# Kernel tuning notes

Hardware: AMD Instinct MI355X
Metric: run time of the kernel (lower is better)

Reference implementation:

```python
import jax, jax.numpy as jnp
import numpy as np

BINS = 2048
DST_NBINS = 8
STEP = 1e-5


def _get_norm(delta_begin, delta_end, density):
    # integral of x^2 * density over [delta_begin, delta_end]
    return density * (delta_end ** 3 - delta_begin ** 3) / 3.0


def _quant_error(hist, bin_width, nsb, neb):
    # L2 quantization error of mapping src bins [nsb, neb] onto DST_NBINS bins
    dst_w = bin_width * (neb - nsb + 1).astype(jnp.float32) / DST_NBINS
    safe_w = jnp.where(dst_w == 0.0, 1.0, dst_w)
    src = jnp.arange(BINS, dtype=jnp.float32)
    begin = (src - nsb) * bin_width          # src bin left edge rel. to new range
    end = begin + bin_width
    db = jnp.clip(jnp.floor(begin / safe_w), 0, DST_NBINS - 1)
    de = jnp.clip(jnp.floor(end / safe_w), 0, DST_NBINS - 1)
    density = hist / bin_width
    db_c = (db + 0.5) * safe_w
    norm = _get_norm(begin - db_c, safe_w / 2, density)
    norm = norm + (de - db - 1.0) * _get_norm(-safe_w / 2, safe_w / 2, density)
    de_c = de * safe_w + safe_w / 2
    norm = norm + _get_norm(-safe_w / 2, end - de_c, density)
    return jnp.where(dst_w == 0.0, jnp.float32(0.0), norm.sum())


def _search(hist, min_val, max_val):
    # entropy-style greedy shrink of [start_bin, end_bin]; sequential, data-dependent
    bin_width = (max_val - min_val) / BINS
    total = hist.sum()
    cSum = jnp.cumsum(hist)

    def cond(s):
        alpha, beta, sb, eb, nm, done = s
        return (alpha < beta) & jnp.logical_not(done)

    def body(s):
        alpha, beta, sb, eb, nm, done = s
        na = alpha + STEP
        nb = beta - STEP
        # l: first bin (>= sb) with cSum >= na*total; r: last bin with cSum <= nb*total
        l = jnp.clip(jnp.searchsorted(cSum, na * total, side='left'), sb, eb)
        r = jnp.clip(jnp.searchsorted(cSum, nb * total, side='right') - 1, sb, eb)
        take_left = (l - sb) > (eb - r)
        nsb = jnp.where(take_left, l, sb)
        neb = jnp.where(take_left, eb, r)
        alpha2 = jnp.where(take_left, na, alpha)
        beta2 = jnp.where(take_left, beta, nb)
        changed = (nsb != sb) | (neb != eb)
        norm = _quant_error(hist, bin_width, nsb, neb)
        broke = changed & (norm > nm)
        accept = changed & jnp.logical_not(broke)
        return (alpha2, beta2,
                jnp.where(accept, nsb, sb),
                jnp.where(accept, neb, eb),
                jnp.where(accept, norm, nm),
                done | broke)

    init = (jnp.float32(0.0), jnp.float32(1.0),
            jnp.int32(0), jnp.int32(BINS - 1),
            jnp.float32(jnp.inf), jnp.bool_(False))
    _, _, sb, eb, _, _ = jax.lax.while_loop(cond, body, init)
    return sb, eb


def _forward(x):
    min_val = jnp.min(x)
    max_val = jnp.max(x)
    bin_width = (max_val - min_val) / BINS
    safe_bw = jnp.where(bin_width == 0.0, 1.0, bin_width)
    # torch.histc equivalent over [min_val, max_val]
    idx = jnp.clip(jnp.floor((x.ravel() - min_val) / safe_bw).astype(jnp.int32), 0, BINS - 1)
    hist = jnp.zeros(BINS, jnp.float32).at[idx].add(1.0)
    sb, eb = _search(jax.lax.stop_gradient(hist),
                     jax.lax.stop_gradient(min_val),
                     jax.lax.stop_gradient(max_val))
    new_min = min_val + bin_width * sb
    new_max = min_val + bin_width * (eb + 1)
    return jnp.stack([new_min, new_max])


def setup_inputs() -> dict:
    key = jax.random.key(0)
    x = jax.random.normal(key, (32, 1024, 1024), dtype=jnp.float32)
    return {"x": x}


def reference(x):
    return _forward(x)
```

## Files before the change

### kernel.cpp

```cpp
#include <hip/hip_runtime.h>
#include <float.h>
#include <math.h>

#define BINS 2048
#define DSTN 8
#define STEPF 1e-5f
#define NPART 1024
#define MAXST 2048
#define NSEG 64
#define MINF 0x7fffffff

struct Ws {
  float pmin[NPART];
  float pmax[NPART];
  float min_val, max_val, bin_width, safe_bw;
  int   n_states;
  int   pad[3];
  unsigned int hist[BINS];
  float histf[BINS];
  float norms[MAXST];
  int2  states[MAXST];
};

__global__ void __launch_bounds__(256) k_minmax(const float* __restrict__ x, long long n,
                                                Ws* __restrict__ ws) {
  long long n4 = n >> 2;
  float vmin = FLT_MAX, vmax = -FLT_MAX;
  const float4* __restrict__ x4 = (const float4*)x;
  long long stride = (long long)gridDim.x * blockDim.x;
  for (long long i = (long long)blockIdx.x * blockDim.x + threadIdx.x; i < n4; i += stride) {
    float4 v = x4[i];
    vmin = fminf(vmin, fminf(fminf(v.x, v.y), fminf(v.z, v.w)));
    vmax = fmaxf(vmax, fmaxf(fmaxf(v.x, v.y), fmaxf(v.z, v.w)));
  }
  for (long long i = (n4 << 2) + (long long)blockIdx.x * blockDim.x + threadIdx.x; i < n; i += stride) {
    float v = x[i];
    vmin = fminf(vmin, v); vmax = fmaxf(vmax, v);
  }
  for (int off = 32; off > 0; off >>= 1) {
    vmin = fminf(vmin, __shfl_down(vmin, off));
    vmax = fmaxf(vmax, __shfl_down(vmax, off));
  }
  __shared__ float smin[4], smax[4];
  int wid = threadIdx.x >> 6;
  if ((threadIdx.x & 63) == 0) { smin[wid] = vmin; smax[wid] = vmax; }
  __syncthreads();
  if (threadIdx.x == 0) {
    float a = smin[0], b = smax[0];
    int nw = (int)(blockDim.x >> 6);
    for (int w = 1; w < nw; ++w) { a = fminf(a, smin[w]); b = fmaxf(b, smax[w]); }
    ws->pmin[blockIdx.x] = a; ws->pmax[blockIdx.x] = b;
  }
}

__global__ void __launch_bounds__(256) k_minmax_final(Ws* __restrict__ ws, int nparts) {
  __shared__ float smin[256], smax[256];
  int t = threadIdx.x;
  float vmin = FLT_MAX, vmax = -FLT_MAX;
  for (int i = t; i < nparts; i += 256) {
    vmin = fminf(vmin, ws->pmin[i]);
    vmax = fmaxf(vmax, ws->pmax[i]);
  }
  smin[t] = vmin; smax[t] = vmax;
  __syncthreads();
  for (int off = 128; off > 0; off >>= 1) {
    if (t < off) { smin[t] = fminf(smin[t], smin[t + off]); smax[t] = fmaxf(smax[t], smax[t + off]); }
    __syncthreads();
  }
  if (t == 0) {
    float mn = smin[0], mx = smax[0];
    ws->min_val = mn; ws->max_val = mx;
    float bw = (mx - mn) / (float)BINS;
    ws->bin_width = bw;
    ws->safe_bw = (bw == 0.0f) ? 1.0f : bw;
  }
  for (int i = t; i < BINS; i += 256) ws->hist[i] = 0u;
}

__global__ void __launch_bounds__(256) k_hist(const float* __restrict__ x, long long n,
                                              Ws* __restrict__ ws) {
  __shared__ unsigned int lh[BINS];
  for (int i = threadIdx.x; i < BINS; i += 256) lh[i] = 0u;
  __syncthreads();
  float minv = ws->min_val;
  float sbw = ws->safe_bw;
  long long n4 = n >> 2;
  const float4* __restrict__ x4 = (const float4*)x;
  long long stride = (long long)gridDim.x * blockDim.x;
  for (long long i = (long long)blockIdx.x * blockDim.x + threadIdx.x; i < n4; i += stride) {
    float4 v = x4[i];
    int a = (int)floorf((v.x - minv) / sbw);
    int b = (int)floorf((v.y - minv) / sbw);
    int c = (int)floorf((v.z - minv) / sbw);
    int d = (int)floorf((v.w - minv) / sbw);
    a = min(BINS - 1, max(0, a));
    b = min(BINS - 1, max(0, b));
    c = min(BINS - 1, max(0, c));
    d = min(BINS - 1, max(0, d));
    atomicAdd(&lh[a], 1u);
    atomicAdd(&lh[b], 1u);
    atomicAdd(&lh[c], 1u);
    atomicAdd(&lh[d], 1u);
  }
  for (long long i = (n4 << 2) + (long long)blockIdx.x * blockDim.x + threadIdx.x; i < n; i += stride) {
    int a = (int)floorf((x[i] - minv) / sbw);
    a = min(BINS - 1, max(0, a));
    atomicAdd(&lh[a], 1u);
  }
  __syncthreads();
  for (int i = threadIdx.x; i < BINS; i += 256) {
    unsigned int c = lh[i];
    if (c) atomicAdd(&ws->hist[i], c);
  }
}

__global__ void __launch_bounds__(256) k_search(Ws* __restrict__ ws) {
  __shared__ __align__(16) char arena[49216];
  float* csum   = (float*)(arena);
  float* Atab   = (float*)(arena + 8192);
  int2*  ev     = (int2*)(arena);
  int2*  ltmt   = (int2*)(arena + 16400);
  int*   mcross = (int*)(arena + 32816);
  int*   chain  = (int*)(arena + 41008);
  __shared__ __align__(16) int2 sstates[MAXST];
  __shared__ float part[256];
  __shared__ int   ipart[256];
  __shared__ int   ipart2[256];
  __shared__ __align__(16) int4 segB4[NSEG];
  __shared__ __align__(16) int4 segA4[NSEG];
  __shared__ int nseg_s, mbot_s, nsegA_s, nc_s;
  __shared__ int pub_mode, pub_j0, pub_sb, pub_mt, pub_nst0;

  int t = threadIdx.x;

  float loc[8];
  float s = 0.0f;
  #pragma unroll
  for (int kk = 0; kk < 8; ++kk) {
    float h = (float)ws->hist[t * 8 + kk];
    ws->histf[t * 8 + kk] = h;
    s += h;
    loc[kk] = s;
  }
  part[t] = s;
  __syncthreads();
  for (int off = 1; off < 256; off <<= 1) {
    float add = (t >= off) ? part[t - off] : 0.0f;
    __syncthreads();
    part[t] += add;
    __syncthreads();
  }
  float excl = (t == 0) ? 0.0f : part[t - 1];
  #pragma unroll
  for (int kk = 0; kk < 8; ++kk) csum[t * 8 + kk] = excl + loc[kk];
  __syncthreads();

  const float S = STEPF;
  const float T = csum[BINS - 1];
  const float rcpT = 1.0f / T;

  if (t == 0) {
    int sg = 0; float B = 1.0f; int m0 = 0; int mbot = MINF;
    while (sg < NSEG && B > 0.0f) {
      float Bn = B - S;
      if (Bn <= 0.0f) {
        segB4[sg] = make_int4(__float_as_int(B), __float_as_int(B - Bn), m0, 0);
        ++sg; mbot = m0 + 1; break;
      }
      float d = B - Bn;
      unsigned bb = __float_as_uint(B);
      unsigned bid = bb & 0x7f800000u;
      if ((bb & 0x007fffffu) == 0u) bid -= 0x00800000u;
      float binlo = __uint_as_float(bid);
      float brel = B - binlo;
      int n = (int)floor((double)brel / (double)d);
      if (n < 0) n = 0;
      if (n >= 2) {
        float B1 = B - d;
        float B2 = B1 - S;
        if (B1 - B2 != d) n = 1;
      }
      segB4[sg] = make_int4(__float_as_int(B), __float_as_int(d), m0, n);
      ++sg;
      float Blast = B - (float)n * d;
      B = Blast - S;
      m0 += n + 1;
      if (B <= 0.0f) { mbot = m0; break; }
    }
    nseg_s = sg; mbot_s = mbot;

    int sa = 0;
    segA4[sa++] = make_int4(__float_as_int(0.0f), __float_as_int(S), 0, 0);
    float A0 = S; int k0 = 1;
    while (sa < NSEG && k0 <= 2051) {
      float An = A0 + S;
      float d = An - A0;
      unsigned ab = __float_as_uint(A0);
      unsigned abid = ab & 0x7f800000u;
      float binhi = __uint_as_float(abid + 0x00800000u);
      float brel = binhi - A0;
      int n = (int)floorf(brel / d);
      if (n < 0) n = 0;
      while (n >= 1 && !(A0 + (float)n * d < binhi)) --n;
      while (A0 + (float)(n + 1) * d < binhi) ++n;
      if (n >= 2) {
        float A1 = A0 + d;
        float A2 = A1 + S;
        if (A2 - A1 != d) n = 1;
      }
      if (k0 + n > 2051) n = 2051 - k0;
      segA4[sa++] = make_int4(__float_as_int(A0), __float_as_int(d), k0, n);
      float Alast = A0 + (float)n * d;
      A0 = Alast + S;
      k0 += n + 1;
    }
    nsegA_s = sa;
  }
  __syncthreads();

  int nsg = nseg_s;
  int mbot = mbot_s;
  int nsa = nsegA_s;

  for (int k = t; k < 2052; k += 256) {
    float val = 0.0f;
    for (int sg = 0; sg < nsa; ++sg) {
      int4 sv = segA4[sg];
      if (k <= sv.z + sv.w) { val = __int_as_float(sv.x) + (float)(k - sv.z) * __int_as_float(sv.y); break; }
    }
    Atab[k] = val;
  }
  __syncthreads();

  {
    int okA = 1;
    for (int k = t; k < 2051; k += 256) okA &= (Atab[k] + S == Atab[k + 1]) ? 1 : 0;
    ipart[t] = okA;
    __syncthreads();
    for (int off = 128; off > 0; off >>= 1) {
      if (t < off) ipart[t] = min(ipart[t], ipart[t + off]);
      __syncthreads();
    }
    if (ipart[0] == 0) {
      if (t == 0) {
        float a = 0.0f; Atab[0] = 0.0f;
        for (int k = 1; k < 2052; ++k) { a = a + S; Atab[k] = a; }
      }
      __syncthreads();
    }
  }

  int lov[9], hiv[9];
  float av1[9];
  #pragma unroll
  for (int i = 0; i < 9; ++i) {
    int k = t + 256 * i;
    lov[i] = 0; hiv[i] = BINS;
    av1[i] = (k <= 2050) ? Atab[k + 1] * T : FLT_MAX;
  }
  #pragma unroll
  for (int lev = 0; lev < 12; ++lev) {
    #pragma unroll
    for (int i = 0; i < 9; ++i) {
      bool act = lov[i] < hiv[i];
      int mid = act ? ((lov[i] + hiv[i]) >> 1) : 0;
      float cv = csum[mid];
      bool g = act && (cv < av1[i]);
      lov[i] = g ? (mid + 1) : lov[i];
      hiv[i] = (act && !g) ? mid : hiv[i];
    }
  }
  #pragma unroll
  for (int i = 0; i < 9; ++i) {
    int k = t + 256 * i;
    if (k >= 2052) break;
    float a = Atab[k];
    int mt = mbot;
    for (int sg = 0; sg < nsg; ++sg) {
      int4 sv = segB4[sg];
      float Bs = __int_as_float(sv.x), dd = __int_as_float(sv.y);
      int ms = sv.z, n = sv.w;
      float Bend = Bs - (float)n * dd;
      if (Bend <= a) {
        float rd = (dd > 0.0f) ? 1.0f / dd : 0.0f;
        int i2 = (int)((Bs - a) * rd);
        if (i2 < 0) i2 = 0; if (i2 > n) i2 = n;
        while (i2 > 0 && Bs - (float)(i2 - 1) * dd <= a) --i2;
        while (i2 <= n && Bs - (float)i2 * dd > a) ++i2;
        mt = ms + i2;
        break;
      }
    }
    ltmt[k] = make_int2(lov[i], mt);
  }
  for (int b = t; b < BINS; b += 256) {
    float c = csum[b];
    int mc = MINF;
    if (c > 0.0f) {
      mc = (mbot == MINF) ? MINF : (mbot - 1);
      for (int sg = 0; sg < nsg; ++sg) {
        int4 sv = segB4[sg];
        float Bs = __int_as_float(sv.x), dd = __int_as_float(sv.y);
        int ms = sv.z, n = sv.w;
        float Bend = Bs - (float)n * dd;
        if (Bend * T < c) {
          float rd = (dd > 0.0f) ? 1.0f / dd : 0.0f;
          int i2 = (int)((Bs - c * rcpT) * rd);
          if (i2 < 0) i2 = 0; if (i2 > n) i2 = n;
          while (i2 > 0 && (Bs - (float)(i2 - 1) * dd) * T < c) --i2;
          while (i2 <= n && !((Bs - (float)i2 * dd) * T < c)) ++i2;
          mc = ms + i2 - 1;
          break;
        }
      }
    }
    mcross[b] = mc;
  }
  __syncthreads();

  int mcl[8];
  int iem = 0;
  {
    int b0 = t * 8;
    #pragma unroll
    for (int kk = 0; kk < 8; ++kk) mcl[kk] = mcross[b0 + kk];
    int mnext = (t < 255) ? mcross[b0 + 8] : 0;
    int cnt = 0;
    #pragma unroll
    for (int kk = 0; kk < 8; ++kk) {
      int nxtv = (kk < 7) ? mcl[kk + 1] : mnext;
      bool e = (b0 + kk == BINS - 1) || (mcl[kk] != nxtv);
      iem |= e ? (1 << kk) : 0;
      cnt += e ? 1 : 0;
    }
    ipart[t] = cnt;
  }
  __syncthreads();
  for (int off = 1; off < 256; off <<= 1) {
    int v = (t + off < 256) ? ipart[t + off] : 0;
    __syncthreads();
    ipart[t] += v;
    __syncthreads();
  }
  {
    int running = (t < 255) ? ipart[t + 1] : 0;
    #pragma unroll
    for (int kk = 7; kk >= 0; --kk) {
      if (iem & (1 << kk)) { ++running; chain[running - 1] = t * 8 + kk; }
    }
    if (t == 0) nc_s = ipart[0];
  }
  __syncthreads();

  int NC = nc_s;
  for (int j = 1 + t; j <= NC; j += 256) {
    int prev = chain[j - 1];
    int mcp = mcross[prev];
    int nxt = (j < NC) ? chain[j] : -1;
    ev[j] = make_int2(mcp, nxt);
  }
  __syncthreads();

  if (t == 0) {
    int k = 0, sb = 0, eb = BINS - 1, m = 0, j = 1, nst = 0;
    int2 lm0 = ltmt[0], lm1 = ltmt[1], lm2 = ltmt[2];
    int2 e0 = ev[1], e1 = ev[2], e2 = ev[3];
    int mode = 0;
    int guard = 0;
    while (++guard < 6000) {
      int lpos = lm0.x, mt = lm0.y;
      int mc = e0.x, ne = e0.y;
      int l = min(lpos, eb);
      int pl = l - sb;
      if (pl <= 0) { mode = 1; pub_j0 = j; pub_sb = sb; pub_mt = mt; break; }
      if (m >= mt) break;
      bool coin = (m == mc);
      int nec = max(ne, sb);
      int pr = eb - nec;
      bool fl = !coin || (pl > pr);
      if (fl) {
        sb = l; ++k;
        sstates[nst] = make_int2(sb, eb); ++nst;
        if (sb >= eb) break;
        lm0 = lm1; lm1 = lm2; lm2 = ltmt[min(k + 2, 2051)];
      } else {
        eb = nec; m = mc + 1; ++j;
        sstates[nst] = make_int2(sb, eb); ++nst;
        if (sb >= eb) break;
        e0 = e1; e1 = e2; e2 = ev[min(j + 2, 2048)];
      }
    }
    pub_mode = mode; pub_nst0 = nst;
    if (mode == 0) { pub_j0 = 0; pub_sb = 0; pub_mt = 0; }
  }
  __syncthreads();

  int mode = pub_mode;
  int nst0 = pub_nst0;
  int ntot = nst0;
  if (mode == 1) {
    int j0 = pub_j0, sbF = pub_sb, mtF = pub_mt;
    int locA = NC + 1, locB = NC + 1;
    for (int j = j0 + t; j <= NC; j += 256) {
      int2 e = ev[j];
      if (e.x >= mtF && j < locA) locA = j;
      if (e.y <= sbF && j < locB) locB = j;
    }
    ipart[t] = locA; ipart2[t] = locB;
    __syncthreads();
    for (int off = 128; off > 0; off >>= 1) {
      if (t < off) {
        ipart[t] = min(ipart[t], ipart[t + off]);
        ipart2[t] = min(ipart2[t], ipart2[t + off]);
      }
      __syncthreads();
    }
    int jA = ipart[0], jB = ipart2[0];
    int nfire, clampLast;
    if (jB < jA) { nfire = jB - j0 + 1; clampLast = 1; }
    else         { nfire = jA - j0;     clampLast = 0; }
    if (nfire < 0) nfire = 0;
    ntot = nst0 + nfire;
    if (ntot > MAXST) ntot = MAXST;
    for (int i = t; i < nfire; i += 256) {
      int idx = nst0 + i;
      if (idx < MAXST) {
        int y = ev[j0 + i].y;
        int ebv = (clampLast && i == nfire - 1) ? sbF : y;
        ws->states[idx] = make_int2(sbF, ebv);
      }
    }
  }
  for (int i = t; i < nst0 && i < MAXST; i += 256) ws->states[i] = sstates[i];
  if (t == 0) ws->n_states = ntot;
}

__global__ void __launch_bounds__(256) k_eval(Ws* __restrict__ ws) {
  int i = blockIdx.x;
  if (i >= ws->n_states) return;
  int2 st = ws->states[i];
  float bw = ws->bin_width;
  float cnt = (float)(st.y - st.x + 1);
  float w = bw * cnt / (float)DSTN;
  int t = threadIdx.x;
  if (w == 0.0f) {
    if (t == 0) ws->norms[i] = 0.0f;
    return;
  }
  float hw = 0.5f * w;
  float hw3 = hw * hw * hw;
  float nsb = (float)st.x;
  float sum = 0.0f;
  #pragma unroll
  for (int k = 0; k < 8; ++k) {
    int j = t + 256 * k;
    float h = ws->histf[j];
    float begin = ((float)j - nsb) * bw;
    float end = begin + bw;
    float db = fminf(fmaxf(floorf(begin / w), 0.0f), (float)(DSTN - 1));
    float de = fminf(fmaxf(floorf(end / w), 0.0f), (float)(DSTN - 1));
    float density = h / bw;
    float dbc = (db + 0.5f) * w;
    float a1 = begin - dbc;
    float n1 = density * (hw3 - a1 * a1 * a1) / 3.0f;
    float nmid = density * (hw3 + hw3) / 3.0f;
    float dec = de * w + hw;
    float a3 = end - dec;
    float n3 = density * (a3 * a3 * a3 + hw3) / 3.0f;
    sum += n1 + (de - db - 1.0f) * nmid + n3;
  }
  __shared__ float red[256];
  red[t] = sum;
  __syncthreads();
  for (int off = 128; off > 0; off >>= 1) {
    if (t < off) red[t] += red[t + off];
    __syncthreads();
  }
  if (t == 0) ws->norms[i] = red[0];
}

__global__ void __launch_bounds__(256) k_final(Ws* __restrict__ ws, float* __restrict__ out) {
  __shared__ int sbrk[256];
  int N = ws->n_states;
  int t = threadIdx.x;
  int loc = 0x7fffffff;
  for (int i = t + 1; i < N; i += 256) {
    if (ws->norms[i] > ws->norms[i - 1]) loc = min(loc, i);
  }
  sbrk[t] = loc;
  __syncthreads();
  for (int off = 128; off > 0; off >>= 1) {
    if (t < off) sbrk[t] = min(sbrk[t], sbrk[t + off]);
    __syncthreads();
  }
  if (t == 0) {
    int sb, eb;
    if (N == 0) { sb = 0; eb = BINS - 1; }
    else {
      int ib = sbrk[0];
      int fi = (ib != 0x7fffffff) ? (ib - 1) : (N - 1);
      int2 st = ws->states[fi];
      sb = st.x; eb = st.y;
    }
    float minv = ws->min_val, bw = ws->bin_width;
    out[0] = minv + bw * (float)sb;
    out[1] = minv + bw * (float)(eb + 1);
  }
}

extern "C" void kernel_launch(void* const* d_in, const int* in_sizes, int n_in,
                              void* d_out, int out_size, void* d_ws, size_t ws_size,
                              hipStream_t stream) {
  const float* x = (const float*)d_in[0];
  long long n = (long long)in_sizes[0];
  Ws* ws = (Ws*)d_ws;
  float* out = (float*)d_out;

  k_minmax<<<NPART, 256, 0, stream>>>(x, n, ws);
  k_minmax_final<<<1, 256, 0, stream>>>(ws, NPART);
  k_hist<<<NPART, 256, 0, stream>>>(x, n, ws);
  k_search<<<1, 256, 0, stream>>>(ws);
  k_eval<<<MAXST, 256, 0, stream>>>(ws);
  k_final<<<1, 256, 0, stream>>>(ws, out);
}
```

Before: 162.8 us.

## Replicate shared histogram bins and widen search kernel with wave-level scans

The histogram kernel now keeps four sub-copies of each bin in shared memory, indexed by thread lane, to cut same-address atomic contention, and merges them with a vector load at the end. The single-block search kernel goes from 256 to 512 threads. It swaps its shared-memory Hillis-Steele scans and tree reductions for wave shuffle scans and __syncthreads_and. Per-segment range bounds are computed up front so each crossing index is computed for only its own range instead of looping over segments. The changes trade 4x shared memory in the histogram (lower occupancy) for less atomic serialization and fewer barriers in the serial search stage.

After: 155.3 us. -4.6%, faster.

```diff
diff --git a/kernel.cpp b/kernel.cpp
--- a/kernel.cpp
+++ b/kernel.cpp
@@ -9,6 +9,7 @@
 #define MAXST 2048
 #define NSEG 64
 #define MINF 0x7fffffff
+#define NT 512
 
 struct Ws {
   float pmin[NPART];
@@ -79,11 +80,12 @@
 
 __global__ void __launch_bounds__(256) k_hist(const float* __restrict__ x, long long n,
                                               Ws* __restrict__ ws) {
-  __shared__ unsigned int lh[BINS];
-  for (int i = threadIdx.x; i < BINS; i += 256) lh[i] = 0u;
+  __shared__ __align__(16) unsigned int lh[BINS * 4];
+  for (int i = threadIdx.x; i < BINS * 4; i += 256) lh[i] = 0u;
   __syncthreads();
   float minv = ws->min_val;
   float sbw = ws->safe_bw;
+  int sub = threadIdx.x & 3;
   long long n4 = n >> 2;
   const float4* __restrict__ x4 = (const float4*)x;
   long long stride = (long long)gridDim.x * blockDim.x;
@@ -97,24 +99,25 @@
     b = min(BINS - 1, max(0, b));
     c = min(BINS - 1, max(0, c));
     d = min(BINS - 1, max(0, d));
-    atomicAdd(&lh[a], 1u);
-    atomicAdd(&lh[b], 1u);
-    atomicAdd(&lh[c], 1u);
-    atomicAdd(&lh[d], 1u);
+    atomicAdd(&lh[(a << 2) | sub], 1u);
+    atomicAdd(&lh[(b << 2) | sub], 1u);
+    atomicAdd(&lh[(c << 2) | sub], 1u);
+    atomicAdd(&lh[(d << 2) | sub], 1u);
   }
   for (long long i = (n4 << 2) + (long long)blockIdx.x * blockDim.x + threadIdx.x; i < n; i += stride) {
     int a = (int)floorf((x[i] - minv) / sbw);
     a = min(BINS - 1, max(0, a));
-    atomicAdd(&lh[a], 1u);
+    atomicAdd(&lh[(a << 2) | sub], 1u);
   }
   __syncthreads();
   for (int i = threadIdx.x; i < BINS; i += 256) {
-    unsigned int c = lh[i];
+    uint4 v = *((const uint4*)lh + i);
+    unsigned int c = v.x + v.y + v.z + v.w;
     if (c) atomicAdd(&ws->hist[i], c);
   }
 }
 
-__global__ void __launch_bounds__(256) k_search(Ws* __restrict__ ws) {
+__global__ void __launch_bounds__(NT) k_search(Ws* __restrict__ ws) {
   __shared__ __align__(16) char arena[49216];
   float* csum   = (float*)(arena);
   float* Atab   = (float*)(arena + 8192);
@@ -123,39 +126,53 @@
   int*   mcross = (int*)(arena + 32816);
   int*   chain  = (int*)(arena + 41008);
   __shared__ __align__(16) int2 sstates[MAXST];
-  __shared__ float part[256];
-  __shared__ int   ipart[256];
-  __shared__ int   ipart2[256];
+  __shared__ float fred[8];
+  __shared__ int   ired[8], ired2[8];
   __shared__ __align__(16) int4 segB4[NSEG];
   __shared__ __align__(16) int4 segA4[NSEG];
+  __shared__ int segklo[NSEG], segblo[NSEG];
   __shared__ int nseg_s, mbot_s, nsegA_s, nc_s;
-  __shared__ int pub_mode, pub_j0, pub_sb, pub_mt, pub_nst0;
+  __shared__ int pub_mode, pub_j0, pub_sb, pub_mt, pub_nst0, pub_nfire, pub_clamp, pub_ntot;
 
   int t = threadIdx.x;
-
-  float loc[8];
+  int lane = t & 63, wid = t >> 6;
+  const float S = STEPF;
+
+  float loc[4];
   float s = 0.0f;
   #pragma unroll
-  for (int kk = 0; kk < 8; ++kk) {
-    float h = (float)ws->hist[t * 8 + kk];
-    ws->histf[t * 8 + kk] = h;
+  for (int kk = 0; kk < 4; ++kk) {
+    float h = (float)ws->hist[t * 4 + kk];
+    ws->histf[t * 4 + kk] = h;
     s += h;
     loc[kk] = s;
   }
-  part[t] = s;
-  __syncthreads();
-  for (int off = 1; off < 256; off <<= 1) {
-    float add = (t >= off) ? part[t - off] : 0.0f;
-    __syncthreads();
-    part[t] += add;
-    __syncthreads();
-  }
-  float excl = (t == 0) ? 0.0f : part[t - 1];
+  float isc = s;
   #pragma unroll
-  for (int kk = 0; kk < 8; ++kk) csum[t * 8 + kk] = excl + loc[kk];
-  __syncthreads();
-
-  const float S = STEPF;
+  for (int off = 1; off < 64; off <<= 1) {
+    float u = __shfl_up(isc, off);
+    if (lane >= off) isc += u;
+  }
+  if (lane == 63) fred[wid] = isc;
+  __syncthreads();
+  if (t < 8) {
+    float v = fred[t];
+    #pragma unroll
+    for (int off = 1; off < 8; off <<= 1) {
+      float u = __shfl_up(v, off, 8);
+      if ((t & 7) >= off) v += u;
+    }
+    fred[t] = v;
+  }
+  __syncthreads();
+  {
+    float base = wid ? fred[wid - 1] : 0.0f;
+    float excl = base + (isc - s);
+    #pragma unroll
+    for (int kk = 0; kk < 4; ++kk) csum[t * 4 + kk] = excl + loc[kk];
+  }
+  __syncthreads();
+
   const float T = csum[BINS - 1];
   const float rcpT = 1.0f / T;
 
@@ -222,26 +239,17 @@
   int mbot = mbot_s;
   int nsa = nsegA_s;
 
-  for (int k = t; k < 2052; k += 256) {
-    float val = 0.0f;
-    for (int sg = 0; sg < nsa; ++sg) {
-      int4 sv = segA4[sg];
-      if (k <= sv.z + sv.w) { val = __int_as_float(sv.x) + (float)(k - sv.z) * __int_as_float(sv.y); break; }
-    }
-    Atab[k] = val;
+  for (int sg = 0; sg < nsa; ++sg) {
+    int4 sv = segA4[sg];
+    float A0v = __int_as_float(sv.x), dv = __int_as_float(sv.y);
+    for (int i = t; i <= sv.w; i += NT) Atab[sv.z + i] = A0v + (float)i * dv;
   }
   __syncthreads();
 
   {
     int okA = 1;
-    for (int k = t; k < 2051; k += 256) okA &= (Atab[k] + S == Atab[k + 1]) ? 1 : 0;
-    ipart[t] = okA;
-    __syncthreads();
-    for (int off = 128; off > 0; off >>= 1) {
-      if (t < off) ipart[t] = min(ipart[t], ipart[t + off]);
-      __syncthreads();
-    }
-    if (ipart[0] == 0) {
+    for (int k = t; k < 2051; k += NT) okA &= (Atab[k] + S == Atab[k + 1]) ? 1 : 0;
+    if (__syncthreads_and(okA) == 0) {
       if (t == 0) {
         float a = 0.0f; Atab[0] = 0.0f;
         for (int k = 1; k < 2052; ++k) { a = a + S; Atab[k] = a; }
@@ -250,115 +258,145 @@
     }
   }
 
-  int lov[9], hiv[9];
-  float av1[9];
-  #pragma unroll
-  for (int i = 0; i < 9; ++i) {
-    int k = t + 256 * i;
-    lov[i] = 0; hiv[i] = BINS;
-    av1[i] = (k <= 2050) ? Atab[k + 1] * T : FLT_MAX;
-  }
-  #pragma unroll
-  for (int lev = 0; lev < 12; ++lev) {
-    #pragma unroll
-    for (int i = 0; i < 9; ++i) {
-      bool act = lov[i] < hiv[i];
-      int mid = act ? ((lov[i] + hiv[i]) >> 1) : 0;
-      float cv = csum[mid];
-      bool g = act && (cv < av1[i]);
-      lov[i] = g ? (mid + 1) : lov[i];
-      hiv[i] = (act && !g) ? mid : hiv[i];
-    }
-  }
-  #pragma unroll
-  for (int i = 0; i < 9; ++i) {
-    int k = t + 256 * i;
-    if (k >= 2052) break;
-    float a = Atab[k];
-    int mt = mbot;
+  {
+    int lov[5], hiv[5];
+    float av1[5];
+    #pragma unroll
+    for (int i = 0; i < 5; ++i) {
+      int k = t + NT * i;
+      lov[i] = 0; hiv[i] = BINS;
+      av1[i] = (k <= 2050) ? Atab[k + 1] * T : FLT_MAX;
+    }
+    #pragma unroll
+    for (int lev = 0; lev < 12; ++lev) {
+      #pragma unroll
+      for (int i = 0; i < 5; ++i) {
+        bool act = lov[i] < hiv[i];
+        int mid = act ? ((lov[i] + hiv[i]) >> 1) : 0;
+        float cv = csum[mid];
+        bool g = act && (cv < av1[i]);
+        lov[i] = g ? (mid + 1) : lov[i];
+        hiv[i] = (act && !g) ? mid : hiv[i];
+      }
+    }
+    #pragma unroll
+    for (int i = 0; i < 5; ++i) {
+      int k = t + NT * i;
+      if (k < 2052) ltmt[k] = make_int2((k <= 2050) ? lov[i] : BINS, 0);
+    }
+  }
+  if (t < nsg) {
+    int4 sv = segB4[t];
+    float Bs = __int_as_float(sv.x), dd = __int_as_float(sv.y);
+    float Bend = Bs - (float)sv.w * dd;
+    int lo = 0, hi = 2052;
+    while (lo < hi) { int mid = (lo + hi) >> 1; if (Atab[mid] < Bend) lo = mid + 1; else hi = mid; }
+    segklo[t] = lo;
+    float vt = Bend * T;
+    lo = 0; hi = BINS;
+    while (lo < hi) { int mid = (lo + hi) >> 1; if (!(csum[mid] > vt)) lo = mid + 1; else hi = mid; }
+    segblo[t] = lo;
+  }
+  __syncthreads();
+
+  {
+    int* ltY = (int*)ltmt;
     for (int sg = 0; sg < nsg; ++sg) {
+      int lo = segklo[sg], hi = (sg ? segklo[sg - 1] : 2052);
+      if (lo >= hi) continue;
       int4 sv = segB4[sg];
       float Bs = __int_as_float(sv.x), dd = __int_as_float(sv.y);
       int ms = sv.z, n = sv.w;
-      float Bend = Bs - (float)n * dd;
-      if (Bend <= a) {
-        float rd = (dd > 0.0f) ? 1.0f / dd : 0.0f;
+      float rd = (dd > 0.0f) ? 1.0f / dd : 0.0f;
+      for (int k = lo + t; k < hi; k += NT) {
+        float a = Atab[k];
         int i2 = (int)((Bs - a) * rd);
         if (i2 < 0) i2 = 0; if (i2 > n) i2 = n;
         while (i2 > 0 && Bs - (float)(i2 - 1) * dd <= a) --i2;
         while (i2 <= n && Bs - (float)i2 * dd > a) ++i2;
-        mt = ms + i2;
-        break;
-      }
-    }
-    ltmt[k] = make_int2(lov[i], mt);
-  }
-  for (int b = t; b < BINS; b += 256) {
-    float c = csum[b];
-    int mc = MINF;
-    if (c > 0.0f) {
-      mc = (mbot == MINF) ? MINF : (mbot - 1);
-      for (int sg = 0; sg < nsg; ++sg) {
-        int4 sv = segB4[sg];
-        float Bs = __int_as_float(sv.x), dd = __int_as_float(sv.y);
-        int ms = sv.z, n = sv.w;
-        float Bend = Bs - (float)n * dd;
-        if (Bend * T < c) {
-          float rd = (dd > 0.0f) ? 1.0f / dd : 0.0f;
-          int i2 = (int)((Bs - c * rcpT) * rd);
-          if (i2 < 0) i2 = 0; if (i2 > n) i2 = n;
-          while (i2 > 0 && (Bs - (float)(i2 - 1) * dd) * T < c) --i2;
-          while (i2 <= n && !((Bs - (float)i2 * dd) * T < c)) ++i2;
-          mc = ms + i2 - 1;
-          break;
-        }
-      }
-    }
-    mcross[b] = mc;
-  }
-  __syncthreads();
-
-  int mcl[8];
-  int iem = 0;
-  {
-    int b0 = t * 8;
-    #pragma unroll
-    for (int kk = 0; kk < 8; ++kk) mcl[kk] = mcross[b0 + kk];
-    int mnext = (t < 255) ? mcross[b0 + 8] : 0;
-    int cnt = 0;
-    #pragma unroll
-    for (int kk = 0; kk < 8; ++kk) {
-      int nxtv = (kk < 7) ? mcl[kk + 1] : mnext;
+        ltY[2 * k + 1] = ms + i2;
+      }
+    }
+    int dhi = segklo[nsg - 1];
+    for (int k = t; k < dhi; k += NT) ltY[2 * k + 1] = mbot;
+  }
+  {
+    for (int sg = 0; sg < nsg; ++sg) {
+      int lo = segblo[sg], hi = (sg ? segblo[sg - 1] : BINS);
+      if (lo >= hi) continue;
+      int4 sv = segB4[sg];
+      float Bs = __int_as_float(sv.x), dd = __int_as_float(sv.y);
+      int ms = sv.z, n = sv.w;
+      float rd = (dd > 0.0f) ? 1.0f / dd : 0.0f;
+      for (int b = lo + t; b < hi; b += NT) {
+        float c = csum[b];
+        int i2 = (int)((Bs - c * rcpT) * rd);
+        if (i2 < 0) i2 = 0; if (i2 > n) i2 = n;
+        while (i2 > 0 && (Bs - (float)(i2 - 1) * dd) * T < c) --i2;
+        while (i2 <= n && !((Bs - (float)i2 * dd) * T < c)) ++i2;
+        mcross[b] = ms + i2 - 1;
+      }
+    }
+    int dhi = segblo[nsg - 1];
+    for (int b = t; b < dhi; b += NT) {
+      float c = csum[b];
+      mcross[b] = (c > 0.0f) ? ((mbot == MINF) ? MINF : (mbot - 1)) : MINF;
+    }
+  }
+  __syncthreads();
+
+  int iem = 0, cnt = 0;
+  {
+    int b0 = t * 4;
+    int mcl[4];
+    #pragma unroll
+    for (int kk = 0; kk < 4; ++kk) mcl[kk] = mcross[b0 + kk];
+    int mnext = (t < NT - 1) ? mcross[b0 + 4] : 0;
+    #pragma unroll
+    for (int kk = 0; kk < 4; ++kk) {
+      int nxtv = (kk < 3) ? mcl[kk + 1] : mnext;
       bool e = (b0 + kk == BINS - 1) || (mcl[kk] != nxtv);
       iem |= e ? (1 << kk) : 0;
       cnt += e ? 1 : 0;
     }
-    ipart[t] = cnt;
-  }
-  __syncthreads();
-  for (int off = 1; off < 256; off <<= 1) {
-    int v = (t + off < 256) ? ipart[t + off] : 0;
-    __syncthreads();
-    ipart[t] += v;
-    __syncthreads();
-  }
-  {
-    int running = (t < 255) ? ipart[t + 1] : 0;
-    #pragma unroll
-    for (int kk = 7; kk >= 0; --kk) {
-      if (iem & (1 << kk)) { ++running; chain[running - 1] = t * 8 + kk; }
-    }
-    if (t == 0) nc_s = ipart[0];
+  }
+  {
+    int inc = cnt;
+    #pragma unroll
+    for (int off = 1; off < 64; off <<= 1) {
+      int u = __shfl_up(inc, off);
+      if (lane >= off) inc += u;
+    }
+    if (lane == 63) ired[wid] = inc;
+    __syncthreads();
+    if (t < 8) {
+      int v = ired[t];
+      #pragma unroll
+      for (int off = 1; off < 8; off <<= 1) {
+        int u = __shfl_up(v, off, 8);
+        if ((t & 7) >= off) v += u;
+      }
+      ired[t] = v;
+    }
+    __syncthreads();
+    int base = wid ? ired[wid - 1] : 0;
+    int incl_t = base + inc;
+    int total = ired[7];
+    int running = total - incl_t;
+    #pragma unroll
+    for (int kk = 3; kk >= 0; --kk) {
+      if (iem & (1 << kk)) { ++running; chain[running - 1] = t * 4 + kk; }
+    }
+    if (t == 0) nc_s = total;
   }
   __syncthreads();
 
   int NC = nc_s;
-  for (int j = 1 + t; j <= NC; j += 256) {
+  for (int j = 1 + t; j <= NC; j += NT) {
     int prev = chain[j - 1];
-    int mcp = mcross[prev];
-    int nxt = (j < NC) ? chain[j] : -1;
-    ev[j] = make_int2(mcp, nxt);
-  }
+    ev[j] = make_int2(mcross[prev], (j < NC) ? chain[j] : -1);
+  }
+  if (t == 0 && NC < 2048) ev[NC + 1] = make_int2(MINF, -1);
   __syncthreads();
 
   if (t == 0) {
@@ -367,6 +405,7 @@
     int2 e0 = ev[1], e1 = ev[2], e2 = ev[3];
     int mode = 0;
     int guard = 0;
+    pub_j0 = 0; pub_sb = 0; pub_mt = 0;
     while (++guard < 6000) {
       int lpos = lm0.x, mt = lm0.y;
       int mc = e0.x, ne = e0.y;
@@ -380,59 +419,65 @@
       bool fl = !coin || (pl > pr);
       if (fl) {
         sb = l; ++k;
-        sstates[nst] = make_int2(sb, eb); ++nst;
+        if (nst < MAXST) sstates[nst] = make_int2(sb, eb);
+        ++nst;
         if (sb >= eb) break;
         lm0 = lm1; lm1 = lm2; lm2 = ltmt[min(k + 2, 2051)];
       } else {
         eb = nec; m = mc + 1; ++j;
-        sstates[nst] = make_int2(sb, eb); ++nst;
+        if (nst < MAXST) sstates[nst] = make_int2(sb, eb);
+        ++nst;
         if (sb >= eb) break;
         e0 = e1; e1 = e2; e2 = ev[min(j + 2, 2048)];
       }
     }
-    pub_mode = mode; pub_nst0 = nst;
-    if (mode == 0) { pub_j0 = 0; pub_sb = 0; pub_mt = 0; }
+    pub_mode = mode;
+    pub_nst0 = (nst < MAXST) ? nst : MAXST;
   }
   __syncthreads();
 
   int mode = pub_mode;
   int nst0 = pub_nst0;
-  int ntot = nst0;
   if (mode == 1) {
     int j0 = pub_j0, sbF = pub_sb, mtF = pub_mt;
     int locA = NC + 1, locB = NC + 1;
-    for (int j = j0 + t; j <= NC; j += 256) {
+    for (int j = j0 + t; j <= NC; j += NT) {
       int2 e = ev[j];
       if (e.x >= mtF && j < locA) locA = j;
       if (e.y <= sbF && j < locB) locB = j;
     }
-    ipart[t] = locA; ipart2[t] = locB;
-    __syncthreads();
-    for (int off = 128; off > 0; off >>= 1) {
-      if (t < off) {
-        ipart[t] = min(ipart[t], ipart[t + off]);
-        ipart2[t] = min(ipart2[t], ipart2[t + off]);
-      }
-      __syncthreads();
-    }
-    int jA = ipart[0], jB = ipart2[0];
-    int nfire, clampLast;
-    if (jB < jA) { nfire = jB - j0 + 1; clampLast = 1; }
-    else         { nfire = jA - j0;     clampLast = 0; }
-    if (nfire < 0) nfire = 0;
-    ntot = nst0 + nfire;
-    if (ntot > MAXST) ntot = MAXST;
-    for (int i = t; i < nfire; i += 256) {
+    #pragma unroll
+    for (int off = 32; off > 0; off >>= 1) {
+      locA = min(locA, __shfl_down(locA, off));
+      locB = min(locB, __shfl_down(locB, off));
+    }
+    if (lane == 0) { ired[wid] = locA; ired2[wid] = locB; }
+    __syncthreads();
+    if (t == 0) {
+      int jA = NC + 1, jB = NC + 1;
+      for (int w = 0; w < 8; ++w) { jA = min(jA, ired[w]); jB = min(jB, ired2[w]); }
+      int nfire, clampLast;
+      if (jB < jA) { nfire = jB - j0 + 1; clampLast = 1; }
+      else         { nfire = jA - j0;     clampLast = 0; }
+      if (nfire < 0) nfire = 0;
+      int ntot = nst0 + nfire;
+      if (ntot > MAXST) ntot = MAXST;
+      pub_nfire = nfire; pub_clamp = clampLast; pub_ntot = ntot;
+    }
+    __syncthreads();
+    int nfire = pub_nfire, clampLast = pub_clamp;
+    for (int i = t; i < nfire; i += NT) {
       int idx = nst0 + i;
       if (idx < MAXST) {
         int y = ev[j0 + i].y;
-        int ebv = (clampLast && i == nfire - 1) ? sbF : y;
-        ws->states[idx] = make_int2(sbF, ebv);
-      }
-    }
-  }
-  for (int i = t; i < nst0 && i < MAXST; i += 256) ws->states[i] = sstates[i];
-  if (t == 0) ws->n_states = ntot;
+        ws->states[idx] = make_int2(sbF, (clampLast && i == nfire - 1) ? sbF : y);
+      }
+    }
+    if (t == 0) ws->n_states = pub_ntot;
+  } else {
+    if (t == 0) ws->n_states = nst0;
+  }
+  for (int i = t; i < nst0; i += NT) ws->states[i] = sstates[i];
 }
 
 __global__ void __launch_bounds__(256) k_eval(Ws* __restrict__ ws) {
@@ -519,7 +564,7 @@
   k_minmax<<<NPART, 256, 0, stream>>>(x, n, ws);
   k_minmax_final<<<1, 256, 0, stream>>>(ws, NPART);
   k_hist<<<NPART, 256, 0, stream>>>(x, n, ws);
-  k_search<<<1, 256, 0, stream>>>(ws);
+  k_search<<<1, NT, 0, stream>>>(ws);
   k_eval<<<MAXST, 256, 0, stream>>>(ws);
   k_final<<<1, 256, 0, stream>>>(ws, out);
 }
```
